# Kernel tuning notes

Measured on AMD Instinct MI355X. Metric: run time of the kernel, lower is better.

Reference implementation:

```python
import jax, jax.numpy as jnp
import numpy as np

HIDDEN = 256
GROUPS = 4
GDIM = HIDDEN // GROUPS  # 64


def setup_inputs() -> dict:
    key = jax.random.key(0)
    k1, k2, k3, k4 = jax.random.split(key, 4)
    B, N, P = 8, 300, 32
    x = jax.random.normal(k1, (B, N, P, HIDDEN), dtype=jnp.float32)
    query_content = jax.random.normal(k2, (B, N, HIDDEN), dtype=jnp.float32)
    out_dim = GDIM * GDIM * GROUPS
    # nn.Linear default init: U(-1/sqrt(fan_in), 1/sqrt(fan_in))
    bound = 1.0 / np.sqrt(HIDDEN)
    W_gen = jax.random.uniform(k3, (HIDDEN, out_dim), dtype=jnp.float32, minval=-bound, maxval=bound)
    b_gen = jax.random.uniform(k4, (out_dim,), dtype=jnp.float32, minval=-bound, maxval=bound)
    gamma = jnp.ones((HIDDEN,), dtype=jnp.float32)
    beta = jnp.zeros((HIDDEN,), dtype=jnp.float32)
    return {"x": x, "query_content": query_content, "W_gen": W_gen, "b_gen": b_gen, "gamma": gamma, "beta": beta}


def _layer_norm(h, gamma, beta, eps=1e-5):
    mu = jnp.mean(h, axis=-1, keepdims=True)
    var = jnp.var(h, axis=-1, keepdims=True)
    return (h - mu) * jax.lax.rsqrt(var + eps) * gamma + beta


def reference(x, query_content, W_gen, b_gen, gamma, beta):
    B, N, P, C = x.shape
    # dynamic per-query weights: [B,N,G,gd,gd]
    w = (query_content @ W_gen + b_gen).reshape(B, N, GROUPS, GDIM, GDIM)
    xg = x.reshape(B, N, P, GROUPS, GDIM)
    # mixed[...,p,g,e] = sum_d xg[...,p,g,d] * w[...,g,e,d]  (matmul with W^T)
    mixed = jnp.einsum('bnpgd,bnged->bnpge', xg, w).reshape(B, N, P, C)
    return jax.nn.relu(_layer_norm(mixed, gamma, beta))
```

## Files before the change

### kernel.cpp

```cpp
#include <hip/hip_runtime.h>
#include <hip/hip_bf16.h>

typedef __attribute__((ext_vector_type(4))) float floatx4;
typedef __attribute__((ext_vector_type(8))) short short8;

#define HIDDEN 256
#define NOUT 16384

static __device__ __forceinline__ short bf16bits(float x) {
    __hip_bfloat16 h = __float2bfloat16(x);
    return __builtin_bit_cast(short, h);
}

#define GLDS16(gsrc, ldst) \
    __builtin_amdgcn_global_load_lds((const __attribute__((address_space(1))) void*)(gsrc), \
                                     (__attribute__((address_space(3))) void*)(ldst), 16, 0, 0)

static __device__ __forceinline__ int permc(int c) {
    const int g = c >> 12, e = (c >> 6) & 63, d = c & 63;
    const int nt = e >> 4, lq = e & 15, ks = (d >> 5) & 1, quad = (d >> 3) & 3, j = d & 7;
    return ((((g << 2) | nt) << 1 | ks) << 9) | (((quad << 4) | lq) << 3) | j;
}
static __device__ __forceinline__ int invperm(int p) {
    const int blk = p >> 9, g = blk >> 3, nt = (blk >> 1) & 3, ks = blk & 1;
    const int r = (p >> 3) & 63, quad = r >> 4, lq = r & 15, j = p & 7;
    return g * 4096 + (nt * 16 + lq) * 64 + ks * 32 + quad * 8 + j;
}

__global__ __launch_bounds__(256) void kPrep(
    const float* __restrict__ Wg, short* __restrict__ WgTp,
    const float* __restrict__ qc, short* __restrict__ qcb, int n4)
{
    __shared__ short t[64 * 68];
    const int tid = threadIdx.x;

    if (blockIdx.x < 1024) {
        const int n0 = (blockIdx.x & 255) * 64, k0 = (blockIdx.x >> 8) * 64;
        const int r  = tid >> 4;
        const int c4 = tid & 15;
        #pragma unroll
        for (int i = 0; i < 4; ++i) {
            const int kl = r + i * 16;
            float4 f = *reinterpret_cast<const float4*>(Wg + (size_t)(k0 + kl) * NOUT + n0 + c4 * 4);
            short4 v;
            v.x = bf16bits(f.x); v.y = bf16bits(f.y); v.z = bf16bits(f.z); v.w = bf16bits(f.w);
            *reinterpret_cast<short4*>(&t[kl * 68 + c4 * 4]) = v;
        }
        __syncthreads();
        #pragma unroll
        for (int h = 0; h < 2; ++h) {
            const int id = tid + h * 256;
            const int nl = id >> 3, kc = id & 7;
            short8 v;
            #pragma unroll
            for (int j = 0; j < 8; ++j) v[j] = t[(kc * 8 + j) * 68 + nl];
            const int prow = permc(n0 + nl);
            *reinterpret_cast<short8*>(WgTp + (size_t)prow * HIDDEN + k0 + kc * 8) = v;
        }
    } else {
        const int i = (blockIdx.x - 1024) * 256 + tid;
        if (i < n4) {
            float4 f = reinterpret_cast<const float4*>(qc)[i];
            short4 v;
            v.x = bf16bits(f.x); v.y = bf16bits(f.y); v.z = bf16bits(f.z); v.w = bf16bits(f.w);
            reinterpret_cast<short4*>(qcb)[i] = v;
        }
    }
}

__global__ __launch_bounds__(256) void kA5(
    const short* __restrict__ qcb, const short* __restrict__ WgTp,
    const float* __restrict__ bg, short* __restrict__ wdyn, int M)
{
    __shared__ short As[128 * 64];
    __shared__ short Bs[128 * 64];

    const int tid  = threadIdx.x;
    const int wave = tid >> 6, lane = tid & 63;
    const int lq   = lane & 15, quad = lane >> 4;
    const int wm   = wave >> 1, wn = wave & 1;
    const int m0   = blockIdx.x * 128;
    const int n0   = blockIdx.y * 128;

    const short* aSrc[4]; const short* bSrc[4];
    short* aDst[4]; short* bDst[4];
    #pragma unroll
    for (int t = 0; t < 4; ++t) {
        const int chunk = t * 256 + wave * 64 + lane;
        const int row = chunk >> 3, kc = chunk & 7;
        const int kcs = kc ^ (row & 7);
        int rA = m0 + row; if (rA >= M) rA = M - 1;
        aSrc[t] = qcb  + (size_t)rA * HIDDEN + kcs * 8;
        bSrc[t] = WgTp + (size_t)(n0 + row) * HIDDEN + kcs * 8;
        aDst[t] = &As[(t * 256 + wave * 64) * 8];
        bDst[t] = &Bs[(t * 256 + wave * 64) * 8];
    }

    int aOff[2][4], bOff[2][4];
    #pragma unroll
    for (int ks = 0; ks < 2; ++ks)
        #pragma unroll
        for (int i = 0; i < 4; ++i) {
            const int ra = wm * 64 + i * 16 + lq;
            aOff[ks][i] = ra * 64 + (((ks * 4 + quad) ^ (ra & 7)) * 8);
            const int rb = wn * 64 + i * 16 + lq;
            bOff[ks][i] = rb * 64 + (((ks * 4 + quad) ^ (rb & 7)) * 8);
        }

    floatx4 acc[4][4];
    #pragma unroll
    for (int i = 0; i < 4; ++i)
        #pragma unroll
        for (int j = 0; j < 4; ++j) acc[i][j] = (floatx4){0.f, 0.f, 0.f, 0.f};

    for (int it = 0; it < 4; ++it) {
        #pragma unroll
        for (int t = 0; t < 4; ++t) {
            GLDS16(aSrc[t], aDst[t]);
            GLDS16(bSrc[t], bDst[t]);
            aSrc[t] += 64; bSrc[t] += 64;
        }
        __syncthreads();

        #pragma unroll
        for (int ks = 0; ks < 2; ++ks) {
            short8 a[4], b[4];
            #pragma unroll
            for (int i = 0; i < 4; ++i) a[i] = *reinterpret_cast<const short8*>(&As[aOff[ks][i]]);
            #pragma unroll
            for (int j = 0; j < 4; ++j) b[j] = *reinterpret_cast<const short8*>(&Bs[bOff[ks][j]]);
            #pragma unroll
            for (int i = 0; i < 4; ++i)
                #pragma unroll
                for (int j = 0; j < 4; ++j)
                    acc[i][j] = __builtin_amdgcn_mfma_f32_16x16x32_bf16(a[i], b[j], acc[i][j], 0, 0, 0);
        }
        __syncthreads();
    }

    float bv[4];
    #pragma unroll
    for (int j = 0; j < 4; ++j) bv[j] = bg[invperm(n0 + wn * 64 + j * 16 + lq)];

    short* Cs = As;
    #pragma unroll
    for (int half = 0; half < 2; ++half) {
        if (half) __syncthreads();
        if (wm == half) {
            #pragma unroll
            for (int j = 0; j < 4; ++j)
                #pragma unroll
                for (int i = 0; i < 4; ++i)
                    #pragma unroll
                    for (int r = 0; r < 4; ++r)
                        Cs[(i * 16 + quad * 4 + r) * 128 + wn * 64 + j * 16 + lq] =
                            bf16bits(acc[i][j][r] + bv[j]);
        }
        __syncthreads();
        #pragma unroll
        for (int t = 0; t < 4; ++t) {
            const int id = t * 256 + tid;
            const int mr = id >> 4, ch = id & 15;
            const int grow = m0 + half * 64 + mr;
            if (grow < M)
                *reinterpret_cast<short8*>(&wdyn[(size_t)grow * NOUT + n0 + ch * 8]) =
                    *reinterpret_cast<const short8*>(&Cs[mr * 128 + ch * 8]);
        }
    }
}

__global__ __launch_bounds__(256) void kB4(
    const float* __restrict__ x, const short* __restrict__ wdyn,
    const float* __restrict__ gamma, const float* __restrict__ beta,
    float* __restrict__ out)
{
    __shared__ float red[2][4][4][2][2];

    const int tid  = threadIdx.x;
    const int bnq  = blockIdx.x;
    const int wave = tid >> 6, lane = tid & 63;
    const int lq   = lane & 15, quad = lane >> 4;
    const int mtile = wave & 1, gp = wave >> 1;

    const float* xr = x + (size_t)bnq * (32 * HIDDEN) + (mtile * 16 + lq) * HIDDEN;
    const short* wr = wdyn + (size_t)bnq * NOUT;

    short8 afr[2][2];
    #pragma unroll
    for (int gi = 0; gi < 2; ++gi) {
        const int g = gp * 2 + gi;
        #pragma unroll
        for (int ks = 0; ks < 2; ++ks) {
            const floatx4* s = reinterpret_cast<const floatx4*>(xr + g * 64 + ks * 32 + quad * 8);
            const floatx4 f0 = __builtin_nontemporal_load(s);
            const floatx4 f1 = __builtin_nontemporal_load(s + 1);
            short8 v;
            v[0]=bf16bits(f0[0]); v[1]=bf16bits(f0[1]); v[2]=bf16bits(f0[2]); v[3]=bf16bits(f0[3]);
            v[4]=bf16bits(f1[0]); v[5]=bf16bits(f1[1]); v[6]=bf16bits(f1[2]); v[7]=bf16bits(f1[3]);
            afr[gi][ks] = v;
        }
    }

    floatx4 acc[2][4];
    #pragma unroll
    for (int gi = 0; gi < 2; ++gi)
        #pragma unroll
        for (int nt = 0; nt < 4; ++nt) acc[gi][nt] = (floatx4){0.f, 0.f, 0.f, 0.f};

    #pragma unroll
    for (int gi = 0; gi < 2; ++gi) {
        const int g = gp * 2 + gi;
        #pragma unroll
        for (int ks = 0; ks < 2; ++ks) {
            #pragma unroll
            for (int nt = 0; nt < 4; ++nt) {
                const short8 b = *reinterpret_cast<const short8*>(
                    wr + (((((g << 2) | nt) << 1) | ks) << 9) + lane * 8);
                acc[gi][nt] = __builtin_amdgcn_mfma_f32_16x16x32_bf16(afr[gi][ks], b, acc[gi][nt], 0, 0, 0);
            }
        }
    }

    float s[4], ss[4];
    #pragma unroll
    for (int r = 0; r < 4; ++r) { s[r] = 0.f; ss[r] = 0.f; }
    #pragma unroll
    for (int gi = 0; gi < 2; ++gi)
        #pragma unroll
        for (int nt = 0; nt < 4; ++nt)
            #pragma unroll
            for (int r = 0; r < 4; ++r) {
                const float v = acc[gi][nt][r];
                s[r] += v; ss[r] += v * v;
            }
    #pragma unroll
    for (int off = 1; off < 16; off <<= 1) {
        #pragma unroll
        for (int r = 0; r < 4; ++r) {
            s[r]  += __shfl_xor(s[r],  off);
            ss[r] += __shfl_xor(ss[r], off);
        }
    }
    if (lq == 0) {
        #pragma unroll
        for (int r = 0; r < 4; ++r) {
            red[mtile][quad][r][gp][0] = s[r];
            red[mtile][quad][r][gp][1] = ss[r];
        }
    }
    __syncthreads();

    float mu[4], rs[4];
    #pragma unroll
    for (int r = 0; r < 4; ++r) {
        const float S  = s[r]  + red[mtile][quad][r][gp ^ 1][0];
        const float SS = ss[r] + red[mtile][quad][r][gp ^ 1][1];
        mu[r] = S * (1.f / 256.f);
        float var = SS * (1.f / 256.f) - mu[r] * mu[r];
        var = fmaxf(var, 0.f);
        rs[r] = rsqrtf(var + 1e-5f);
    }

    float* orow = out + (size_t)bnq * (32 * HIDDEN);
    #pragma unroll
    for (int gi = 0; gi < 2; ++gi) {
        const int g = gp * 2 + gi;
        #pragma unroll
        for (int nt = 0; nt < 4; ++nt) {
            const int c = g * 64 + nt * 16 + lq;
            const float gm = gamma[c], bt = beta[c];
            #pragma unroll
            for (int r = 0; r < 4; ++r) {
                const int p = mtile * 16 + quad * 4 + r;
                const float v = fmaxf((acc[gi][nt][r] - mu[r]) * rs[r] * gm + bt, 0.f);
                __builtin_nontemporal_store(v, &orow[p * HIDDEN + c]);
            }
        }
    }
}

extern "C" void kernel_launch(void* const* d_in, const int* in_sizes, int n_in,
                              void* d_out, int out_size, void* d_ws, size_t ws_size,
                              hipStream_t stream)
{
    const float* x     = (const float*)d_in[0];
    const float* qc    = (const float*)d_in[1];
    const float* Wg    = (const float*)d_in[2];
    const float* bg    = (const float*)d_in[3];
    const float* gamma = (const float*)d_in[4];
    const float* beta  = (const float*)d_in[5];
    float* out = (float*)d_out;

    const int M = in_sizes[1] / HIDDEN;

    char* ws = (char*)d_ws;
    short* wdyn = (short*)ws;
    short* WgTp = (short*)(ws + (size_t)M * NOUT * 2);
    short* qcb  = (short*)(ws + (size_t)M * NOUT * 2 + (size_t)NOUT * HIDDEN * 2);

    const int n4 = (M * HIDDEN) / 4;
    const int prepBlocks = 1024 + (n4 + 255) / 256;
    kPrep<<<prepBlocks, 256, 0, stream>>>(Wg, WgTp, qc, qcb, n4);

    kA5<<<dim3((M + 127) / 128, NOUT / 128), 256, 0, stream>>>(qcb, WgTp, bg, wdyn, M);

    kB4<<<M, 256, 0, stream>>>(x, wdyn, gamma, beta, out);
}
```

Baseline: 220.4 us.

## Swap MFMA operands so each lane owns a row, vectorize LayerNorm stores

The MFMA A/B operands are swapped so each lane's accumulator holds four consecutive channels of a single row rather than four rows. This turns the per-element scalar output stores into 16-byte vector stores and vectorizes the gamma/beta loads. It also shrinks the row-statistics reduction to two cross-quad shuffles with a single mean/rstd per lane. All dynamic-weight fragment loads are hoisted ahead of the x conversion, which raises memory-level parallelism at the cost of more live registers.

```diff
diff --git a/kernel.cpp b/kernel.cpp
--- a/kernel.cpp
+++ b/kernel.cpp
@@ -169,12 +169,12 @@
     }
 }
 
-__global__ __launch_bounds__(256) void kB4(
+__global__ __launch_bounds__(256) void kB5(
     const float* __restrict__ x, const short* __restrict__ wdyn,
     const float* __restrict__ gamma, const float* __restrict__ beta,
     float* __restrict__ out)
 {
-    __shared__ float red[2][4][4][2][2];
+    __shared__ float red[2][2][16][2];
 
     const int tid  = threadIdx.x;
     const int bnq  = blockIdx.x;
@@ -183,23 +183,44 @@
     const int mtile = wave & 1, gp = wave >> 1;
 
     const float* xr = x + (size_t)bnq * (32 * HIDDEN) + (mtile * 16 + lq) * HIDDEN;
-    const short* wr = wdyn + (size_t)bnq * NOUT;
-
-    short8 afr[2][2];
+    const short* wr = wdyn + (size_t)bnq * NOUT + lane * 8;
+
+    floatx4 xf[2][2][2];
     #pragma unroll
     for (int gi = 0; gi < 2; ++gi) {
         const int g = gp * 2 + gi;
         #pragma unroll
         for (int ks = 0; ks < 2; ++ks) {
             const floatx4* s = reinterpret_cast<const floatx4*>(xr + g * 64 + ks * 32 + quad * 8);
-            const floatx4 f0 = __builtin_nontemporal_load(s);
-            const floatx4 f1 = __builtin_nontemporal_load(s + 1);
+            xf[gi][ks][0] = __builtin_nontemporal_load(s);
+            xf[gi][ks][1] = __builtin_nontemporal_load(s + 1);
+        }
+    }
+
+    short8 bfr[2][2][4];
+    #pragma unroll
+    for (int gi = 0; gi < 2; ++gi) {
+        const int g = gp * 2 + gi;
+        #pragma unroll
+        for (int ks = 0; ks < 2; ++ks)
+            #pragma unroll
+            for (int nt = 0; nt < 4; ++nt)
+                bfr[gi][ks][nt] = *reinterpret_cast<const short8*>(
+                    wr + (((((g << 2) | nt) << 1) | ks) << 9));
+    }
+
+    short8 afr[2][2];
+    #pragma unroll
+    for (int gi = 0; gi < 2; ++gi)
+        #pragma unroll
+        for (int ks = 0; ks < 2; ++ks) {
+            const floatx4 f0 = xf[gi][ks][0];
+            const floatx4 f1 = xf[gi][ks][1];
             short8 v;
             v[0]=bf16bits(f0[0]); v[1]=bf16bits(f0[1]); v[2]=bf16bits(f0[2]); v[3]=bf16bits(f0[3]);
             v[4]=bf16bits(f1[0]); v[5]=bf16bits(f1[1]); v[6]=bf16bits(f1[2]); v[7]=bf16bits(f1[3]);
             afr[gi][ks] = v;
         }
-    }
 
     floatx4 acc[2][4];
     #pragma unroll
@@ -207,74 +228,52 @@
         #pragma unroll
         for (int nt = 0; nt < 4; ++nt) acc[gi][nt] = (floatx4){0.f, 0.f, 0.f, 0.f};
 
+    #pragma unroll
+    for (int gi = 0; gi < 2; ++gi)
+        #pragma unroll
+        for (int ks = 0; ks < 2; ++ks)
+            #pragma unroll
+            for (int nt = 0; nt < 4; ++nt)
+                acc[gi][nt] = __builtin_amdgcn_mfma_f32_16x16x32_bf16(
+                    bfr[gi][ks][nt], afr[gi][ks], acc[gi][nt], 0, 0, 0);
+
+    float s = 0.f, ss = 0.f;
+    #pragma unroll
+    for (int gi = 0; gi < 2; ++gi)
+        #pragma unroll
+        for (int nt = 0; nt < 4; ++nt)
+            #pragma unroll
+            for (int r = 0; r < 4; ++r) {
+                const float v = acc[gi][nt][r];
+                s += v; ss += v * v;
+            }
+    s  += __shfl_xor(s, 16);  ss += __shfl_xor(ss, 16);
+    s  += __shfl_xor(s, 32);  ss += __shfl_xor(ss, 32);
+
+    if (quad == 0) { red[mtile][gp][lq][0] = s; red[mtile][gp][lq][1] = ss; }
+    __syncthreads();
+
+    const float S  = s  + red[mtile][gp ^ 1][lq][0];
+    const float SS = ss + red[mtile][gp ^ 1][lq][1];
+    const float mu = S * (1.f / 256.f);
+    float var = SS * (1.f / 256.f) - mu * mu;
+    var = fmaxf(var, 0.f);
+    const float rs = rsqrtf(var + 1e-5f);
+
+    float* orow = out + (size_t)bnq * (32 * HIDDEN) + (mtile * 16 + lq) * HIDDEN;
     #pragma unroll
     for (int gi = 0; gi < 2; ++gi) {
         const int g = gp * 2 + gi;
         #pragma unroll
-        for (int ks = 0; ks < 2; ++ks) {
-            #pragma unroll
-            for (int nt = 0; nt < 4; ++nt) {
-                const short8 b = *reinterpret_cast<const short8*>(
-                    wr + (((((g << 2) | nt) << 1) | ks) << 9) + lane * 8);
-                acc[gi][nt] = __builtin_amdgcn_mfma_f32_16x16x32_bf16(afr[gi][ks], b, acc[gi][nt], 0, 0, 0);
-            }
-        }
-    }
-
-    float s[4], ss[4];
-    #pragma unroll
-    for (int r = 0; r < 4; ++r) { s[r] = 0.f; ss[r] = 0.f; }
-    #pragma unroll
-    for (int gi = 0; gi < 2; ++gi)
-        #pragma unroll
-        for (int nt = 0; nt < 4; ++nt)
-            #pragma unroll
-            for (int r = 0; r < 4; ++r) {
-                const float v = acc[gi][nt][r];
-                s[r] += v; ss[r] += v * v;
-            }
-    #pragma unroll
-    for (int off = 1; off < 16; off <<= 1) {
-        #pragma unroll
-        for (int r = 0; r < 4; ++r) {
-            s[r]  += __shfl_xor(s[r],  off);
-            ss[r] += __shfl_xor(ss[r], off);
-        }
-    }
-    if (lq == 0) {
-        #pragma unroll
-        for (int r = 0; r < 4; ++r) {
-            red[mtile][quad][r][gp][0] = s[r];
-            red[mtile][quad][r][gp][1] = ss[r];
-        }
-    }
-    __syncthreads();
-
-    float mu[4], rs[4];
-    #pragma unroll
-    for (int r = 0; r < 4; ++r) {
-        const float S  = s[r]  + red[mtile][quad][r][gp ^ 1][0];
-        const float SS = ss[r] + red[mtile][quad][r][gp ^ 1][1];
-        mu[r] = S * (1.f / 256.f);
-        float var = SS * (1.f / 256.f) - mu[r] * mu[r];
-        var = fmaxf(var, 0.f);
-        rs[r] = rsqrtf(var + 1e-5f);
-    }
-
-    float* orow = out + (size_t)bnq * (32 * HIDDEN);
-    #pragma unroll
-    for (int gi = 0; gi < 2; ++gi) {
-        const int g = gp * 2 + gi;
-        #pragma unroll
         for (int nt = 0; nt < 4; ++nt) {
-            const int c = g * 64 + nt * 16 + lq;
-            const float gm = gamma[c], bt = beta[c];
-            #pragma unroll
-            for (int r = 0; r < 4; ++r) {
-                const int p = mtile * 16 + quad * 4 + r;
-                const float v = fmaxf((acc[gi][nt][r] - mu[r]) * rs[r] * gm + bt, 0.f);
-                __builtin_nontemporal_store(v, &orow[p * HIDDEN + c]);
-            }
+            const int c0 = g * 64 + nt * 16 + quad * 4;
+            const floatx4 gm = *reinterpret_cast<const floatx4*>(gamma + c0);
+            const floatx4 bt = *reinterpret_cast<const floatx4*>(beta + c0);
+            floatx4 o;
+            #pragma unroll
+            for (int r = 0; r < 4; ++r)
+                o[r] = fmaxf((acc[gi][nt][r] - mu) * rs * gm[r] + bt[r], 0.f);
+            __builtin_nontemporal_store(o, reinterpret_cast<floatx4*>(orow + c0));
         }
     }
 }
@@ -304,5 +303,5 @@
 
     kA5<<<dim3((M + 127) / 128, NOUT / 128), 256, 0, stream>>>(qcb, WgTp, bg, wdyn, M);
 
-    kB4<<<M, 256, 0, stream>>>(x, wdyn, gamma, beta, out);
-}
+    kB5<<<M, 256, 0, stream>>>(x, wdyn, gamma, beta, out);
+}
```

After: 223.0 us. Within noise of the previous version (+1.2%).
